# Kernel tuning notes

Measured on AMD Instinct MI355X. Metric: run time of the kernel, lower is better.

## Reference

```python
import jax, jax.numpy as jnp
import numpy as np

BATCH = 4096
FEAT = 1024
HID = 1024


def setup_inputs() -> dict:
    key = jax.random.key(0)
    ks = jax.random.split(key, 11)
    s_x = 1.0 / np.sqrt(FEAT)
    s_h = 1.0 / np.sqrt(HID)
    return {
        "x": jax.random.normal(ks[0], (BATCH, FEAT), jnp.float32),
        "h_prev": jax.random.normal(ks[1], (BATCH, HID), jnp.float32),
        "c_prev": jax.random.normal(ks[2], (BATCH, HID), jnp.float32),
        # Dense(3*hidden) on x and h (keras Dense: y = x @ W + b)
        "W_ifo_x": jax.random.normal(ks[3], (FEAT, 3 * HID), jnp.float32) * s_x,
        "b_ifo_x": jnp.zeros((3 * HID,), jnp.float32),
        "W_ifo_h": jax.random.normal(ks[4], (HID, 3 * HID), jnp.float32) * s_h,
        "b_ifo_h": jnp.zeros((3 * HID,), jnp.float32),
        # Dense(hidden) on x and h for candidate 'a'
        "W_b_x": jax.random.normal(ks[5], (FEAT, HID), jnp.float32) * s_x,
        "b_b_x": jnp.zeros((HID,), jnp.float32),
        "W_b_h": jax.random.normal(ks[6], (HID, HID), jnp.float32) * s_h,
        "b_b_h": jnp.zeros((HID,), jnp.float32),
    }


def reference(x, h_prev, c_prev, W_ifo_x, b_ifo_x, W_ifo_h, b_ifo_h,
              W_b_x, b_b_x, W_b_h, b_b_h):
    # Fused gate projections: [B, 3H]
    ifo = jax.nn.sigmoid(x @ W_ifo_x + b_ifo_x + h_prev @ W_ifo_h + b_ifo_h)
    i, f, o = jnp.split(ifo, 3, axis=-1)
    a = jnp.tanh(x @ W_b_x + b_b_x + h_prev @ W_b_h + b_b_h)
    c = i * a + f * c_prev
    h = o * jnp.tanh(c)
    return (h, c)
```

## Files before the change

kernel.cpp:

```cpp
#include <hip/hip_runtime.h>
#include <hip/hip_bf16.h>
#include <stdint.h>
#include <stddef.h>


#define BATCH 4096
#define FEAT  1024
#define HID   1024
#define NCAT  4096
#define KCAT  2048

typedef __attribute__((ext_vector_type(8))) __bf16 bf16x8;
typedef __attribute__((ext_vector_type(4))) float  floatx4;

__device__ __forceinline__ unsigned short f2bf(float f) {
    __hip_bfloat16 b = __float2bfloat16(f);
    return *reinterpret_cast<unsigned short*>(&b);
}
__device__ __forceinline__ void gl2lds16(const unsigned short* g, unsigned short* l) {
    __builtin_amdgcn_global_load_lds(
        (const __attribute__((address_space(1))) void*)g,
        (__attribute__((address_space(3))) void*)l, 16, 0, 0);
}

__global__ __launch_bounds__(256)
void xh_pack(const float* __restrict__ x, const float* __restrict__ h,
             unsigned short* __restrict__ Xcat) {
    const int t = threadIdx.x;
    const int m = blockIdx.x;
    const float* src = (t < 128) ? (x + (size_t)m * FEAT + t * 8)
                                 : (h + (size_t)m * HID + (t - 128) * 8);
    float4 v0 = *(const float4*)src;
    float4 v1 = *(const float4*)(src + 4);
    union { unsigned short s16[8]; uint4 v; } pk;
    pk.s16[0] = f2bf(v0.x); pk.s16[1] = f2bf(v0.y);
    pk.s16[2] = f2bf(v0.z); pk.s16[3] = f2bf(v0.w);
    pk.s16[4] = f2bf(v1.x); pk.s16[5] = f2bf(v1.y);
    pk.s16[6] = f2bf(v1.z); pk.s16[7] = f2bf(v1.w);
    *(uint4*)(Xcat + (size_t)m * KCAT + t * 8) = pk.v;
}

#define TP_PAD 65
__global__ __launch_bounds__(256)
void wt_pack(const float* __restrict__ Wix, const float* __restrict__ Wih,
             const float* __restrict__ Wbx, const float* __restrict__ Wbh,
             unsigned short* __restrict__ Wt) {
    __shared__ unsigned short tile[64 * TP_PAD];
    const int t  = threadIdx.x;
    const int k0 = blockIdx.x * 64;
    const int q0 = blockIdx.y * 64;
    const float* src; int stride, cb;
    if (q0 < 3072) { src = (k0 < FEAT) ? Wix : Wih; stride = 3072; cb = q0; }
    else           { src = (k0 < FEAT) ? Wbx : Wbh; stride = 1024; cb = q0 - 3072; }
    const int krow = (k0 < FEAT) ? k0 : (k0 - FEAT);
    {
        int kl = t >> 2;
        int c0 = (t & 3) * 16;
        const float* s = src + (size_t)(krow + kl) * stride + cb + c0;
        unsigned short tmp[16];
#pragma unroll
        for (int u = 0; u < 16; u += 4) {
            float4 v = *(const float4*)(s + u);
            tmp[u + 0] = f2bf(v.x); tmp[u + 1] = f2bf(v.y);
            tmp[u + 2] = f2bf(v.z); tmp[u + 3] = f2bf(v.w);
        }
#pragma unroll
        for (int u = 0; u < 16; ++u) tile[kl * TP_PAD + c0 + u] = tmp[u];
    }
    __syncthreads();
    {
        int nl = t >> 2, seg = t & 3;
        int q = q0 + nl;
        int g, j;
        if (q < 3072) { g = q >> 10; j = q & 1023; }
        else          { g = 3;       j = q - 3072; }
        int np = ((j >> 4) << 6) + (g << 4) + (j & 15);
        union { unsigned short s16[16]; uint4 v[2]; } pk;
#pragma unroll
        for (int u = 0; u < 16; ++u)
            pk.s16[u] = tile[(seg * 16 + u) * TP_PAD + nl];
        uint4* dst = (uint4*)(Wt + (size_t)np * KCAT + k0 + seg * 16);
        dst[0] = pk.v[0];
        dst[1] = pk.v[1];
    }
}

#define BM 128
#define BN 128
#define BK 32

__global__ __launch_bounds__(256)
void lstm_fused(const unsigned short* __restrict__ Xcat,
                const unsigned short* __restrict__ Wt,
                const float* __restrict__ c_prev,
                const float* __restrict__ bix, const float* __restrict__ bih,
                const float* __restrict__ bbx, const float* __restrict__ bbh,
                float* __restrict__ out_h, float* __restrict__ out_c) {
    __shared__ unsigned short As[BM * BK];
    __shared__ unsigned short Bs[BN * BK];
    const int t    = threadIdx.x;
    const int lane = t & 63;
    const int wave = t >> 6;
    const int wm   = (wave >> 1) * 64;
    const int wn   = (wave & 1) * 64;
    const int m0   = blockIdx.y * BM;
    const int n0   = blockIdx.x * BN;

    floatx4 acc[4][4];
#pragma unroll
    for (int i = 0; i < 4; ++i)
#pragma unroll
        for (int g = 0; g < 4; ++g) acc[i][g] = (floatx4){0.f, 0.f, 0.f, 0.f};

    const int lrow = t >> 2;
    const int lcol = (t & 3) * 8;

    for (int kk = 0; kk < KCAT; kk += BK) {
        __syncthreads();
        gl2lds16(Xcat + (size_t)(m0 + lrow)      * KCAT + kk + lcol, &As[t * 8]);
        gl2lds16(Xcat + (size_t)(m0 + lrow + 64) * KCAT + kk + lcol, &As[t * 8 + 2048]);
        gl2lds16(Wt   + (size_t)(n0 + lrow)      * KCAT + kk + lcol, &Bs[t * 8]);
        gl2lds16(Wt   + (size_t)(n0 + lrow + 64) * KCAT + kk + lcol, &Bs[t * 8 + 2048]);
        __syncthreads();

        const int lm = lane & 15;
        const int lk = (lane >> 4) * 8;
        bf16x8 a[4], b[4];
#pragma unroll
        for (int i = 0; i < 4; ++i)
            a[i] = *(const bf16x8*)&As[(wm + i * 16 + lm) * BK + lk];
#pragma unroll
        for (int g = 0; g < 4; ++g)
            b[g] = *(const bf16x8*)&Bs[(wn + g * 16 + lm) * BK + lk];
#pragma unroll
        for (int i = 0; i < 4; ++i)
#pragma unroll
            for (int g = 0; g < 4; ++g)
                acc[i][g] = __builtin_amdgcn_mfma_f32_16x16x32_bf16(a[i], b[g], acc[i][g], 0, 0, 0);
    }

    const int lm = lane & 15;
    const int j  = (((n0 + wn) >> 6) << 4) + lm;
    const float bi = bix[j]           + bih[j];
    const float bf = bix[HID + j]     + bih[HID + j];
    const float bo = bix[2 * HID + j] + bih[2 * HID + j];
    const float ba = bbx[j]           + bbh[j];
#pragma unroll
    for (int i = 0; i < 4; ++i) {
#pragma unroll
        for (int r = 0; r < 4; ++r) {
            int m = m0 + wm + i * 16 + ((lane >> 4) * 4) + r;
            float pi = acc[i][0][r] + bi;
            float pf = acc[i][1][r] + bf;
            float po = acc[i][2][r] + bo;
            float pa = acc[i][3][r] + ba;
            float ig = 1.f / (1.f + __expf(-pi));
            float fg = 1.f / (1.f + __expf(-pf));
            float og = 1.f / (1.f + __expf(-po));
            float av = 2.f / (1.f + __expf(-2.f * pa)) - 1.f;
            float cp = c_prev[(size_t)m * HID + j];
            float cv = ig * av + fg * cp;
            float hv = og * (2.f / (1.f + __expf(-2.f * cv)) - 1.f);
            out_h[(size_t)m * HID + j] = hv;
            out_c[(size_t)m * HID + j] = cv;
        }
    }
}

__global__ void naive_lstm(const float* __restrict__ x, const float* __restrict__ h,
                           const float* __restrict__ cvp,
                           const float* __restrict__ Wix, const float* __restrict__ bix,
                           const float* __restrict__ Wih, const float* __restrict__ bih,
                           const float* __restrict__ Wbx, const float* __restrict__ bbx,
                           const float* __restrict__ Wbh, const float* __restrict__ bbh,
                           float* __restrict__ out_h, float* __restrict__ out_c) {
    const int j = blockIdx.x * 256 + threadIdx.x;
    const int m = blockIdx.y;
    float ai = 0.f, af = 0.f, ao = 0.f, aa = 0.f;
    for (int k = 0; k < FEAT; ++k) {
        float xk = x[(size_t)m * FEAT + k];
        ai += xk * Wix[(size_t)k * 3072 + j];
        af += xk * Wix[(size_t)k * 3072 + HID + j];
        ao += xk * Wix[(size_t)k * 3072 + 2 * HID + j];
        aa += xk * Wbx[(size_t)k * HID + j];
    }
    for (int k = 0; k < HID; ++k) {
        float hk = h[(size_t)m * HID + k];
        ai += hk * Wih[(size_t)k * 3072 + j];
        af += hk * Wih[(size_t)k * 3072 + HID + j];
        ao += hk * Wih[(size_t)k * 3072 + 2 * HID + j];
        aa += hk * Wbh[(size_t)k * HID + j];
    }
    ai += bix[j] + bih[j];
    af += bix[HID + j] + bih[HID + j];
    ao += bix[2 * HID + j] + bih[2 * HID + j];
    aa += bbx[j] + bbh[j];
    float ig = 1.f / (1.f + __expf(-ai));
    float fg = 1.f / (1.f + __expf(-af));
    float og = 1.f / (1.f + __expf(-ao));
    float av = 2.f / (1.f + __expf(-2.f * aa)) - 1.f;
    float cp = cvp[(size_t)m * HID + j];
    float cc = ig * av + fg * cp;
    float hh = og * (2.f / (1.f + __expf(-2.f * cc)) - 1.f);
    out_h[(size_t)m * HID + j] = hh;
    out_c[(size_t)m * HID + j] = cc;
}

extern "C" void kernel_launch(void* const* d_in, const int* in_sizes, int n_in,
                              void* d_out, int out_size, void* d_ws, size_t ws_size,
                              hipStream_t stream) {
    const float* x   = (const float*)d_in[0];
    const float* h   = (const float*)d_in[1];
    const float* c   = (const float*)d_in[2];
    const float* Wix = (const float*)d_in[3];
    const float* bix = (const float*)d_in[4];
    const float* Wih = (const float*)d_in[5];
    const float* bih = (const float*)d_in[6];
    const float* Wbx = (const float*)d_in[7];
    const float* bbx = (const float*)d_in[8];
    const float* Wbh = (const float*)d_in[9];
    const float* bbh = (const float*)d_in[10];

    float* out_h = (float*)d_out;
    float* out_c = out_h + (size_t)BATCH * HID;

    const size_t WT_BYTES = (size_t)NCAT * KCAT * 2;
    const size_t XC_BYTES = (size_t)BATCH * KCAT * 2;
    if (ws_size >= WT_BYTES + XC_BYTES) {
        unsigned short* Wt   = (unsigned short*)d_ws;
        unsigned short* Xcat = (unsigned short*)((char*)d_ws + WT_BYTES);
        xh_pack<<<BATCH, 256, 0, stream>>>(x, h, Xcat);
        wt_pack<<<dim3(KCAT / 64, NCAT / 64), 256, 0, stream>>>(Wix, Wih, Wbx, Wbh, Wt);
        lstm_fused<<<dim3(NCAT / BN, BATCH / BM), 256, 0, stream>>>(
            Xcat, Wt, c, bix, bih, bbx, bbh, out_h, out_c);
    } else {
        naive_lstm<<<dim3(HID / 256, BATCH), 256, 0, stream>>>(
            x, h, c, Wix, bix, Wih, bih, Wbx, bbx, Wbh, bbh, out_h, out_c);
    }
}
```

Measured before the change: 231.0 us.

## Merge pack kernels and XOR-swizzle LDS chunks in GEMM tiles

Merges the activation and weight packing kernels into one launch, with block index selecting the role. The weight transpose tile padding moves to 72 so each thread can write its 16 values to LDS as two 16-byte stores. The GEMM now XOR-swizzles which 8-element k-chunk each row loads from global memory, and the fragment reads apply the matching swizzle, to avoid LDS bank conflicts. This saves one launch and should cut LDS conflict stalls, but it adds index arithmetic and relies on the swizzle keeping each fragment's k-ordering consistent between A and B.

```diff
diff --git a/kernel.cpp b/kernel.cpp
--- a/kernel.cpp
+++ b/kernel.cpp
@@ -23,32 +23,32 @@
         (__attribute__((address_space(3))) void*)l, 16, 0, 0);
 }
 
+#define TP_PAD 72
 __global__ __launch_bounds__(256)
-void xh_pack(const float* __restrict__ x, const float* __restrict__ h,
-             unsigned short* __restrict__ Xcat) {
+void pack_all(const float* __restrict__ x, const float* __restrict__ h,
+              const float* __restrict__ Wix, const float* __restrict__ Wih,
+              const float* __restrict__ Wbx, const float* __restrict__ Wbh,
+              unsigned short* __restrict__ Xcat, unsigned short* __restrict__ Wt) {
+    __shared__ unsigned short tile[64 * TP_PAD];
     const int t = threadIdx.x;
-    const int m = blockIdx.x;
-    const float* src = (t < 128) ? (x + (size_t)m * FEAT + t * 8)
-                                 : (h + (size_t)m * HID + (t - 128) * 8);
-    float4 v0 = *(const float4*)src;
-    float4 v1 = *(const float4*)(src + 4);
-    union { unsigned short s16[8]; uint4 v; } pk;
-    pk.s16[0] = f2bf(v0.x); pk.s16[1] = f2bf(v0.y);
-    pk.s16[2] = f2bf(v0.z); pk.s16[3] = f2bf(v0.w);
-    pk.s16[4] = f2bf(v1.x); pk.s16[5] = f2bf(v1.y);
-    pk.s16[6] = f2bf(v1.z); pk.s16[7] = f2bf(v1.w);
-    *(uint4*)(Xcat + (size_t)m * KCAT + t * 8) = pk.v;
-}
-
-#define TP_PAD 65
-__global__ __launch_bounds__(256)
-void wt_pack(const float* __restrict__ Wix, const float* __restrict__ Wih,
-             const float* __restrict__ Wbx, const float* __restrict__ Wbh,
-             unsigned short* __restrict__ Wt) {
-    __shared__ unsigned short tile[64 * TP_PAD];
-    const int t  = threadIdx.x;
-    const int k0 = blockIdx.x * 64;
-    const int q0 = blockIdx.y * 64;
+    const int b = blockIdx.x;
+    if (b < BATCH) {
+        const int m = b;
+        const float* src = (t < 128) ? (x + (size_t)m * FEAT + t * 8)
+                                     : (h + (size_t)m * HID + (t - 128) * 8);
+        float4 v0 = *(const float4*)src;
+        float4 v1 = *(const float4*)(src + 4);
+        union { unsigned short s16[8]; uint4 v; } pk;
+        pk.s16[0] = f2bf(v0.x); pk.s16[1] = f2bf(v0.y);
+        pk.s16[2] = f2bf(v0.z); pk.s16[3] = f2bf(v0.w);
+        pk.s16[4] = f2bf(v1.x); pk.s16[5] = f2bf(v1.y);
+        pk.s16[6] = f2bf(v1.z); pk.s16[7] = f2bf(v1.w);
+        *(uint4*)(Xcat + (size_t)m * KCAT + t * 8) = pk.v;
+        return;
+    }
+    const int tid = b - BATCH;
+    const int k0  = (tid & 31) * 64;
+    const int q0  = (tid >> 5) * 64;
     const float* src; int stride, cb;
     if (q0 < 3072) { src = (k0 < FEAT) ? Wix : Wih; stride = 3072; cb = q0; }
     else           { src = (k0 < FEAT) ? Wbx : Wbh; stride = 1024; cb = q0 - 3072; }
@@ -57,15 +57,15 @@
         int kl = t >> 2;
         int c0 = (t & 3) * 16;
         const float* s = src + (size_t)(krow + kl) * stride + cb + c0;
-        unsigned short tmp[16];
+        union { unsigned short s16[16]; uint4 v[2]; } tmp;
 #pragma unroll
         for (int u = 0; u < 16; u += 4) {
             float4 v = *(const float4*)(s + u);
-            tmp[u + 0] = f2bf(v.x); tmp[u + 1] = f2bf(v.y);
-            tmp[u + 2] = f2bf(v.z); tmp[u + 3] = f2bf(v.w);
+            tmp.s16[u + 0] = f2bf(v.x); tmp.s16[u + 1] = f2bf(v.y);
+            tmp.s16[u + 2] = f2bf(v.z); tmp.s16[u + 3] = f2bf(v.w);
         }
-#pragma unroll
-        for (int u = 0; u < 16; ++u) tile[kl * TP_PAD + c0 + u] = tmp[u];
+        *(uint4*)&tile[kl * TP_PAD + c0]     = tmp.v[0];
+        *(uint4*)&tile[kl * TP_PAD + c0 + 8] = tmp.v[1];
     }
     __syncthreads();
     {
@@ -113,7 +113,11 @@
         for (int g = 0; g < 4; ++g) acc[i][g] = (floatx4){0.f, 0.f, 0.f, 0.f};
 
     const int lrow = t >> 2;
-    const int lcol = (t & 3) * 8;
+    const int cg   = ((t & 3) ^ (lrow + (lrow >> 2))) & 3;
+    const int lcol = cg * 8;
+
+    const int lm  = lane & 15;
+    const int fcs = ((lane >> 4) ^ (lm + (lm >> 2))) & 3;
 
     for (int kk = 0; kk < KCAT; kk += BK) {
         __syncthreads();
@@ -123,15 +127,13 @@
         gl2lds16(Wt   + (size_t)(n0 + lrow + 64) * KCAT + kk + lcol, &Bs[t * 8 + 2048]);
         __syncthreads();
 
-        const int lm = lane & 15;
-        const int lk = (lane >> 4) * 8;
         bf16x8 a[4], b[4];
 #pragma unroll
         for (int i = 0; i < 4; ++i)
-            a[i] = *(const bf16x8*)&As[(wm + i * 16 + lm) * BK + lk];
+            a[i] = *(const bf16x8*)&As[(wm + i * 16 + lm) * BK + fcs * 8];
 #pragma unroll
         for (int g = 0; g < 4; ++g)
-            b[g] = *(const bf16x8*)&Bs[(wn + g * 16 + lm) * BK + lk];
+            b[g] = *(const bf16x8*)&Bs[(wn + g * 16 + lm) * BK + fcs * 8];
 #pragma unroll
         for (int i = 0; i < 4; ++i)
 #pragma unroll
@@ -139,7 +141,6 @@
                 acc[i][g] = __builtin_amdgcn_mfma_f32_16x16x32_bf16(a[i], b[g], acc[i][g], 0, 0, 0);
     }
 
-    const int lm = lane & 15;
     const int j  = (((n0 + wn) >> 6) << 4) + lm;
     const float bi = bix[j]           + bih[j];
     const float bf = bix[HID + j]     + bih[HID + j];
@@ -229,8 +230,7 @@
     if (ws_size >= WT_BYTES + XC_BYTES) {
         unsigned short* Wt   = (unsigned short*)d_ws;
         unsigned short* Xcat = (unsigned short*)((char*)d_ws + WT_BYTES);
-        xh_pack<<<BATCH, 256, 0, stream>>>(x, h, Xcat);
-        wt_pack<<<dim3(KCAT / 64, NCAT / 64), 256, 0, stream>>>(Wix, Wih, Wbx, Wbh, Wt);
+        pack_all<<<BATCH + 2048, 256, 0, stream>>>(x, h, Wix, Wih, Wbx, Wbh, Xcat, Wt);
         lstm_fused<<<dim3(NCAT / BN, BATCH / BM), 256, 0, stream>>>(
             Xcat, Wt, c, bix, bih, bbx, bbh, out_h, out_c);
     } else {
```

New measurement: 228.8 us. Within noise of the previous version (-0.9%).
